# Kernel optimization log

Measured on AMD Instinct MI355X. Metric: run time of the kernel, lower is better.

Reference implementation:

```python
import jax, jax.numpy as jnp
import numpy as np

H = 64
VOCAB = 64
READ_FREQ = 16


def setup_inputs() -> dict:
    key = jax.random.key(0)
    ks = jax.random.split(key, 16)
    B, L, M = 512, 2048, 256
    seq = jax.random.randint(ks[0], (B, L), 0, VOCAB)
    memory = jax.random.normal(ks[1], (B, M, H), dtype=jnp.float32)
    s = 0.1
    return {
        "seq": seq,
        "memory": memory,
        "embed_w": jax.random.normal(ks[2], (VOCAB, H), jnp.float32) * s,
        "gru_w_ih": jax.random.normal(ks[3], (3 * H, 2 * H), jnp.float32) * s,
        "gru_w_hh": jax.random.normal(ks[4], (3 * H, H), jnp.float32) * s,
        "gru_b_ih": jax.random.normal(ks[5], (3 * H,), jnp.float32) * s,
        "gru_b_hh": jax.random.normal(ks[6], (3 * H,), jnp.float32) * s,
        "key_w": jax.random.normal(ks[7], (H, H), jnp.float32) * s,
        "key_b": jax.random.normal(ks[8], (H,), jnp.float32) * s,
        "val_w": jax.random.normal(ks[9], (H, H), jnp.float32) * s,
        "val_b": jax.random.normal(ks[10], (H,), jnp.float32) * s,
        "query_w": jax.random.normal(ks[11], (H, H), jnp.float32) * s,
        "query_b": jax.random.normal(ks[12], (H,), jnp.float32) * s,
        "head_w": jax.random.normal(ks[13], (VOCAB, H), jnp.float32) * s,
        "head_b": jax.random.normal(ks[14], (VOCAB,), jnp.float32) * s,
    }


def _forward(seq, memory, embed_w, gru_w_ih, gru_w_hh, gru_b_ih, gru_b_hh,
             key_w, key_b, val_w, val_b, query_w, query_b, head_w, head_b):
    B, L = seq.shape
    scale = 1.0 / (H ** 0.5)
    # memory is fixed: precompute keys/values once (B, M, H)
    k = jnp.einsum("bmh,kh->bmk", memory, key_w) + key_b
    v = jnp.einsum("bmh,kh->bmk", memory, val_w) + val_b
    # embed all tokens up front: (B, L, H) -> chunks (C, F, B, H)
    emb = embed_w[seq]
    C = L // READ_FREQ
    emb_chunks = emb.reshape(B, C, READ_FREQ, H).transpose(1, 2, 0, 3)

    def gru_step(carry, x_t):
        h, retrieved = carry
        inp = jnp.concatenate([x_t, retrieved], axis=-1)  # (B, 2H)
        gi = inp @ gru_w_ih.T + gru_b_ih                   # (B, 3H)
        gh = h @ gru_w_hh.T + gru_b_hh                     # (B, 3H)
        i_r, i_z, i_n = jnp.split(gi, 3, axis=-1)
        h_r, h_z, h_n = jnp.split(gh, 3, axis=-1)
        r = jax.nn.sigmoid(i_r + h_r)
        z = jax.nn.sigmoid(i_z + h_z)
        n = jnp.tanh(i_n + r * h_n)
        h_new = (1.0 - z) * n + z * h
        return (h_new, retrieved), None

    def chunk_step(h, chunk_emb):  # chunk_emb: (READ_FREQ, B, H)
        q = h @ query_w.T + query_b                        # (B, H)
        scores = jnp.einsum("bh,bmh->bm", q, k) * scale
        w = jax.nn.softmax(scores, axis=-1)
        retrieved = jnp.einsum("bm,bmh->bh", w, v)
        (h, _), _ = jax.lax.scan(gru_step, (h, retrieved), chunk_emb)
        return h, None

    h0 = jnp.zeros((B, H), dtype=memory.dtype)
    h, _ = jax.lax.scan(chunk_step, h0, emb_chunks)
    return h @ head_w.T + head_b                            # (B, VOCAB)


def reference(seq, memory, embed_w, gru_w_ih, gru_w_hh, gru_b_ih, gru_b_hh,
              key_w, key_b, val_w, val_b, query_w, query_b, head_w, head_b):
    return _forward(seq, memory, embed_w, gru_w_ih, gru_w_hh, gru_b_ih, gru_b_hh,
                    key_w, key_b, val_w, val_b, query_w, query_b, head_w, head_b)
```

## Files before the change

kernel.cpp:

```cpp
#include <hip/hip_runtime.h>
#include <hip/hip_fp16.h>


#define B_ 512
#define L_ 2048
#define M_ 256
#define H_ 64
#define C_ 128
#define F_ 16

typedef float v2f __attribute__((ext_vector_type(2)));
typedef _Float16 h2v __attribute__((ext_vector_type(2)));

#if __has_builtin(__builtin_amdgcn_fdot2)
__device__ __forceinline__ float FDOT2(h2v a, h2v b, float c) {
    return __builtin_amdgcn_fdot2(a, b, c, false);
}
#else
__device__ __forceinline__ float FDOT2(h2v a, h2v b, float c) {
    return c + (float)a[0]*(float)b[0] + (float)a[1]*(float)b[1];
}
#endif

__device__ __forceinline__ h2v bch(unsigned u) { return __builtin_bit_cast(h2v, u); }
__device__ __forceinline__ unsigned rl_u(unsigned v, int lane) {
    return (unsigned)__builtin_amdgcn_readlane((int)v, lane);
}
__device__ __forceinline__ float rl(float v, int lane) {
    return __int_as_float(__builtin_amdgcn_readlane(__float_as_int(v), lane));
}
__device__ __forceinline__ unsigned packpair(float mine, float other, bool odd) {
    float lo = odd ? other : mine;
    float hi = odd ? mine : other;
    auto r = __builtin_amdgcn_cvt_pkrtz(lo, hi);
    return __builtin_bit_cast(unsigned, r);
}
__device__ __forceinline__ float dot4(float4 a, float4 b) {
    return a.x*b.x + a.y*b.y + a.z*b.z + a.w*b.w;
}
__device__ __forceinline__ void cvt2v(uint2 raw, v2f& lo, v2f& hi) {
    __half2* hp = (__half2*)&raw;
    float2 a = __half22float2(hp[0]);
    float2 b = __half22float2(hp[1]);
    lo[0] = a.x; lo[1] = a.y; hi[0] = b.x; hi[1] = b.y;
}
__device__ __forceinline__ float fast_rcp(float x) { return __builtin_amdgcn_rcpf(x); }
__device__ __forceinline__ float sigm(float x) { return fast_rcp(1.f + __expf(-x)); }
__device__ __forceinline__ float tanh_f(float x) {
    float e2 = __expf(-2.f * fabsf(x));
    return copysignf((1.f - e2) * fast_rcp(1.f + e2), x);
}
__device__ __forceinline__ unsigned h2rn(float a, float b) {
    __half2 h = __floats2half2_rn(a, b);
    return __builtin_bit_cast(unsigned, h);
}

#define WS_KT    0u
#define WS_V     16777216u
#define WS_G     33554432u
#define WS_WPHH  33603584u
#define WS_WR    33628160u
#define WS_QP    33652736u
#define WS_KWP   33660928u
#define WS_VWP   33677312u

#define S_KT   0u
#define S_V    32768u
#define S_QP   65536u
#define S_P    73728u
#define SMEM_BYTES 74752u

__global__ void pack_weights(const float* __restrict__ w_ih,
                             const float* __restrict__ w_hh,
                             const float* __restrict__ qw,
                             const float* __restrict__ kw,
                             const float* __restrict__ vw,
                             unsigned* __restrict__ WPhh2,
                             unsigned* __restrict__ WR2p,
                             unsigned* __restrict__ QP2,
                             float4* __restrict__ KWP,
                             float4* __restrict__ VWP)
{
    int idx = blockIdx.x * 256 + threadIdx.x;
    if (idx < 6144) {
        int j = idx & 63, t = idx >> 6, g = t % 3, k2 = t / 3;
        const float* s = w_hh + (g*64 + j)*64 + 2*k2;
        WPhh2[idx] = h2rn(s[0], s[1]);
    } else if (idx < 12288) {
        int i = idx - 6144;
        int j = i & 63, t = i >> 6, g = t % 3, k2 = t / 3;
        const float* s = w_ih + (g*64 + j)*128 + 64 + 2*k2;
        WR2p[i] = h2rn(s[0], s[1]);
    } else if (idx < 14336) {
        int i = idx - 12288;
        int j = i & 63, k2 = i >> 6;
        const float* s = qw + j*64 + 2*k2;
        QP2[i] = h2rn(s[0], s[1]);
    } else if (idx < 15360) {
        int i = idx - 14336;
        int j = i & 63, k4 = i >> 6;
        const float* s = kw + j*64 + 4*k4;
        KWP[i] = make_float4(s[0], s[1], s[2], s[3]);
    } else if (idx < 16384) {
        int i = idx - 15360;
        int j = i & 63, k4 = i >> 6;
        const float* s = vw + j*64 + 4*k4;
        VWP[i] = make_float4(s[0], s[1], s[2], s[3]);
    }
}

__global__ __launch_bounds__(64) void build_G(const float* __restrict__ embed_w,
                                              const float* __restrict__ w_ih,
                                              const float* __restrict__ b_ih,
                                              float* __restrict__ G)
{
    int v = blockIdx.x, j = threadIdx.x;
    __shared__ float e_s[64];
    e_s[j] = embed_w[v*64 + j];
    __syncthreads();
    float a0 = b_ih[j], a1 = b_ih[64 + j], a2 = b_ih[128 + j];
    for (int k = 0; k < 64; ++k) {
        float e = e_s[k];
        a0 += e * w_ih[j*128 + k];
        a1 += e * w_ih[(64 + j)*128 + k];
        a2 += e * w_ih[(128 + j)*128 + k];
    }
    G[v*192 + j]       = a0;
    G[v*192 + 64 + j]  = a1;
    G[v*192 + 128 + j] = a2;
}

__global__ __launch_bounds__(256) void compute_kv(const float* __restrict__ memory,
                                                  const float* __restrict__ key_b,
                                                  const float* __restrict__ val_b,
                                                  const float4* __restrict__ KWP,
                                                  const float4* __restrict__ VWP,
                                                  unsigned* __restrict__ kT2,
                                                  __half* __restrict__ v_h)
{
    int wid = threadIdx.x >> 6;
    int o   = threadIdx.x & 63;
    int row = blockIdx.x * 4 + wid;
    int b = row >> 8, m = row & 255;
    __shared__ __align__(16) float mem_s[4][64];
    mem_s[wid][o] = memory[(size_t)row * 64 + o];
    __syncthreads();
    float ak = key_b[o], av = val_b[o];
    const float4* m4 = (const float4*)mem_s[wid];
#pragma unroll
    for (int k4 = 0; k4 < 16; ++k4) {
        float4 mm = m4[k4];
        ak += dot4(mm, KWP[k4*64 + o]);
        av += dot4(mm, VWP[k4*64 + o]);
    }
    float nb = __shfl_xor(ak, 1);
    if ((o & 1) == 0)
        kT2[((size_t)b*32 + (o >> 1))*256 + m] = h2rn(ak, nb);
    v_h[(size_t)row*64 + o] = __float2half(av);
}

#define GRU_STEP(cg0, cg1, cg2) do {                                        \
    float gr = (cg0) + RrB, gz = (cg1) + RzB, gn = bhn;                     \
    _Pragma("unroll")                                                       \
    for (int kp = 0; kp < 32; ++kp) {                                       \
        h2v hhp = bch(rl_u(hpu, 2*kp));                                     \
        gr = FDOT2(hhp, wr2[kp], gr);                                       \
        gz = FDOT2(hhp, wz2[kp], gz);                                       \
        gn = FDOT2(hhp, wn2[kp], gn);                                       \
    }                                                                       \
    float r_ = sigm(gr);                                                    \
    float z_ = sigm(gz);                                                    \
    float n_ = tanh_f(((cg2) + Rn) + r_ * gn);                              \
    h = fmaf(z_, h - n_, n_);                                               \
    float hx_ = __shfl_xor(h, 1);                                           \
    hpu = packpair(h, hx_, odd);                                            \
} while (0)

__global__ __launch_bounds__(64, 1) void recurrent_main(
    const int*   __restrict__ seq,
    const float* __restrict__ b_hh,
    const float* __restrict__ query_b,
    const float* __restrict__ head_w,
    const float* __restrict__ head_b,
    const unsigned* __restrict__ kT2g,
    const __half* __restrict__ v_h,
    const float* __restrict__ G,
    const unsigned* __restrict__ WPhh2,
    const unsigned* __restrict__ WR2p,
    const unsigned* __restrict__ QP2g,
    float* __restrict__ out)
{
    const int b = blockIdx.x;
    const int j = threadIdx.x;
    const bool odd = (j & 1);

    extern __shared__ __align__(16) char smem[];
    const uint4* kT2_lds = (const uint4*)(smem + S_KT);
    const uint2* v_u2    = (const uint2*)(smem + S_V);
    const unsigned* qp2  = (const unsigned*)(smem + S_QP);
    float4* p_s4  = (float4*)(smem + S_P);

    {
        const uint4* kTg = (const uint4*)(kT2g + (size_t)b * 8192);
        const uint4* vg  = (const uint4*)(v_h  + (size_t)b * 16384);
        uint4* kTls = (uint4*)(smem + S_KT);
        uint4* vls  = (uint4*)(smem + S_V);
#pragma unroll
        for (int i = 0; i < 32; ++i) {
            kTls[i*64 + j] = kTg[i*64 + j];
            vls[i*64 + j]  = vg[i*64 + j];
        }
        const uint4* qpg = (const uint4*)QP2g;
        uint4* qls = (uint4*)(smem + S_QP);
#pragma unroll
        for (int i = 0; i < 8; ++i) qls[i*64 + j] = qpg[i*64 + j];
    }

    h2v wr2[32], wz2[32], wn2[32];
#pragma unroll
    for (int k2 = 0; k2 < 32; ++k2) {
        wr2[k2] = bch(WPhh2[(k2*3 + 0)*64 + j]);
        wz2[k2] = bch(WPhh2[(k2*3 + 1)*64 + j]);
        wn2[k2] = bch(WPhh2[(k2*3 + 2)*64 + j]);
    }
    h2v rr2[32], rz2[32], rn2[32];
#pragma unroll
    for (int k2 = 0; k2 < 32; ++k2) {
        rr2[k2] = bch(WR2p[(k2*3 + 0)*64 + j]);
        rz2[k2] = bch(WR2p[(k2*3 + 1)*64 + j]);
        rn2[k2] = bch(WR2p[(k2*3 + 2)*64 + j]);
    }

    float h = 0.f;
    unsigned hpu = 0u;
    const float bhr = b_hh[j], bhz = b_hh[64 + j], bhn = b_hh[128 + j];
    const float qb  = query_b[j];

    const int* seqb = seq + (size_t)b * L_;
    const int o4 = j & 15;
    const int mg = j >> 4;
    __builtin_amdgcn_wave_barrier();

    for (int c = 0; c < C_; ++c) {
        const int c16 = c * F_;

        float q = qb;
#pragma unroll 8
        for (int k2 = 0; k2 < 32; ++k2) {
            h2v pp = bch(qp2[k2*64 + j]);
            h2v hh = bch(rl_u(hpu, 2*k2));
            q = FDOT2(hh, pp, q);
        }

        float qx = __shfl_xor(q, 1);
        unsigned qpu = packpair(q, qx, odd);
        float s0 = 0.f, s1 = 0.f, s2 = 0.f, s3 = 0.f;
#pragma unroll 8
        for (int t = 0; t < 32; ++t) {
            h2v qq = bch(rl_u(qpu, 2*t));
            uint4 kk = kT2_lds[t*64 + j];
            s0 = FDOT2(bch(kk.x), qq, s0);
            s1 = FDOT2(bch(kk.y), qq, s1);
            s2 = FDOT2(bch(kk.z), qq, s2);
            s3 = FDOT2(bch(kk.w), qq, s3);
        }
        const float scale = 0.125f;
        float4 p;
        p.x = __expf(s0*scale); p.y = __expf(s1*scale);
        p.z = __expf(s2*scale); p.w = __expf(s3*scale);
        float sum = (p.x + p.y) + (p.z + p.w);
#pragma unroll
        for (int o = 32; o > 0; o >>= 1) sum += __shfl_xor(sum, o);
        float inv = fast_rcp(sum);
        p_s4[j] = p;
        __builtin_amdgcn_wave_barrier();

        const float* ps = (const float*)p_s4;
        v2f aA0 = {0.f,0.f}, aB0 = {0.f,0.f};
        v2f aA1 = {0.f,0.f}, aB1 = {0.f,0.f};
#pragma unroll 4
        for (int i = 0; i < 64; i += 2) {
            int m0 = 4*i + mg, m1 = 4*(i + 1) + mg;
            float p0 = ps[m0], p1 = ps[m1];
            v2f v0l, v0h, v1l, v1h;
            cvt2v(v_u2[m0*16 + o4], v0l, v0h);
            cvt2v(v_u2[m1*16 + o4], v1l, v1h);
            aA0 += v0l * p0; aB0 += v0h * p0;
            aA1 += v1l * p1; aB1 += v1h * p1;
        }
        float4 acc;
        acc.x = (aA0[0] + aA1[0]) * inv;
        acc.y = (aA0[1] + aA1[1]) * inv;
        acc.z = (aB0[0] + aB1[0]) * inv;
        acc.w = (aB0[1] + aB1[1]) * inv;
#pragma unroll
        for (int o = 16; o <= 32; o <<= 1) {
            acc.x += __shfl_xor(acc.x, o);
            acc.y += __shfl_xor(acc.y, o);
            acc.z += __shfl_xor(acc.z, o);
            acc.w += __shfl_xor(acc.w, o);
        }

        unsigned rp0 = packpair(acc.x, acc.y, false);
        unsigned rp1 = packpair(acc.z, acc.w, false);
        float Rr = 0.f, Rz = 0.f, Rn = 0.f;
#pragma unroll
        for (int k2 = 0; k2 < 32; ++k2) {
            unsigned rsel = (k2 & 1) ? rp1 : rp0;
            h2v rr = bch(rl_u(rsel, k2 >> 1));
            Rr = FDOT2(rr, rr2[k2], Rr);
            Rz = FDOT2(rr, rz2[k2], Rz);
            Rn = FDOT2(rr, rn2[k2], Rn);
        }
        const float RrB = Rr + bhr, RzB = Rz + bhz;

#pragma unroll 1
        for (int g = 0; g < 4; ++g) {
            const int4 tg = *(const int4*)(seqb + c16 + 4*g);
            const float* GA = G + tg.x*192;
            const float* GB = G + tg.y*192;
            const float* GC = G + tg.z*192;
            const float* GD = G + tg.w*192;
            float gA0 = GA[j], gA1 = GA[64+j], gA2 = GA[128+j];
            float gB0 = GB[j], gB1 = GB[64+j], gB2 = GB[128+j];
            float gC0 = GC[j], gC1 = GC[64+j], gC2 = GC[128+j];
            float gD0 = GD[j], gD1 = GD[64+j], gD2 = GD[128+j];

            GRU_STEP(gA0, gA1, gA2);
            GRU_STEP(gB0, gB1, gB2);
            GRU_STEP(gC0, gC1, gC2);
            GRU_STEP(gD0, gD1, gD2);
        }
    }

    float o = head_b[j];
#pragma unroll
    for (int k4 = 0; k4 < 16; ++k4) {
        float h0 = rl(h, 4*k4+0), h1 = rl(h, 4*k4+1);
        float h2 = rl(h, 4*k4+2), h3 = rl(h, 4*k4+3);
        const float* hw = head_w + j*64 + 4*k4;
        o += h0*hw[0] + h1*hw[1] + h2*hw[2] + h3*hw[3];
    }
    out[(size_t)b*64 + j] = o;
}

extern "C" void kernel_launch(void* const* d_in, const int* in_sizes, int n_in,
                              void* d_out, int out_size, void* d_ws, size_t ws_size,
                              hipStream_t stream) {
    const int*   seq      = (const int*)  d_in[0];
    const float* memory   = (const float*)d_in[1];
    const float* embed_w  = (const float*)d_in[2];
    const float* w_ih     = (const float*)d_in[3];
    const float* w_hh     = (const float*)d_in[4];
    const float* b_ih     = (const float*)d_in[5];
    const float* b_hh     = (const float*)d_in[6];
    const float* key_w    = (const float*)d_in[7];
    const float* key_b    = (const float*)d_in[8];
    const float* val_w    = (const float*)d_in[9];
    const float* val_b    = (const float*)d_in[10];
    const float* query_w  = (const float*)d_in[11];
    const float* query_b  = (const float*)d_in[12];
    const float* head_w   = (const float*)d_in[13];
    const float* head_b   = (const float*)d_in[14];

    char* ws = (char*)d_ws;
    unsigned* kT2  = (unsigned*)(ws + WS_KT);
    __half*   v_h  = (__half*)  (ws + WS_V);
    float*    G    = (float*)   (ws + WS_G);
    unsigned* WPhh2 = (unsigned*)(ws + WS_WPHH);
    unsigned* WR2p  = (unsigned*)(ws + WS_WR);
    unsigned* QP2   = (unsigned*)(ws + WS_QP);
    float4*   KWP   = (float4*)  (ws + WS_KWP);
    float4*   VWP   = (float4*)  (ws + WS_VWP);

    (void)hipFuncSetAttribute((const void*)recurrent_main,
                              hipFuncAttributeMaxDynamicSharedMemorySize,
                              (int)SMEM_BYTES);

    pack_weights<<<64, 256, 0, stream>>>(w_ih, w_hh, query_w, key_w, val_w,
                                         WPhh2, WR2p, QP2, KWP, VWP);
    build_G<<<64, 64, 0, stream>>>(embed_w, w_ih, b_ih, G);
    compute_kv<<<(B_*M_)/4, 256, 0, stream>>>(memory, key_b, val_b, KWP, VWP, kT2, v_h);
    recurrent_main<<<B_, 64, SMEM_BYTES, stream>>>(seq, b_hh, query_b, head_w, head_b,
                                                   kT2, v_h, G, WPhh2, WR2p, QP2,
                                                   (float*)d_out);
}
```

Before: 1.502 ms.

## Transpose values to per-output-row fp16 pairs and use fdot2 for retrieval

Values are now stored transposed, with pairs of memory slots packed as fp16 along m for each output channel. Each lane then computes its own retrieved channel with fdot2 over 256 slots, reading a padded LDS row and a packed fp16 probability vector. This replaces the split-m accumulation that needed cross-lane shuffle reductions and fp16-to-fp32 conversions. Token indices for the chunk are also loaded up front. In exchange, probabilities lose precision by being rounded to fp16, and compute_kv gains an extra block barrier.

```diff
diff --git a/kernel.cpp b/kernel.cpp
--- a/kernel.cpp
+++ b/kernel.cpp
@@ -35,14 +35,12 @@
     auto r = __builtin_amdgcn_cvt_pkrtz(lo, hi);
     return __builtin_bit_cast(unsigned, r);
 }
+__device__ __forceinline__ unsigned pkrtz(float a, float b) {
+    auto r = __builtin_amdgcn_cvt_pkrtz(a, b);
+    return __builtin_bit_cast(unsigned, r);
+}
 __device__ __forceinline__ float dot4(float4 a, float4 b) {
     return a.x*b.x + a.y*b.y + a.z*b.z + a.w*b.w;
-}
-__device__ __forceinline__ void cvt2v(uint2 raw, v2f& lo, v2f& hi) {
-    __half2* hp = (__half2*)&raw;
-    float2 a = __half22float2(hp[0]);
-    float2 b = __half22float2(hp[1]);
-    lo[0] = a.x; lo[1] = a.y; hi[0] = b.x; hi[1] = b.y;
 }
 __device__ __forceinline__ float fast_rcp(float x) { return __builtin_amdgcn_rcpf(x); }
 __device__ __forceinline__ float sigm(float x) { return fast_rcp(1.f + __expf(-x)); }
@@ -66,9 +64,9 @@
 
 #define S_KT   0u
 #define S_V    32768u
-#define S_QP   65536u
-#define S_P    73728u
-#define SMEM_BYTES 74752u
+#define S_QP   66560u
+#define S_P    74752u
+#define SMEM_BYTES 75264u
 
 __global__ void pack_weights(const float* __restrict__ w_ih,
                              const float* __restrict__ w_hh,
@@ -136,13 +134,14 @@
                                                   const float4* __restrict__ KWP,
                                                   const float4* __restrict__ VWP,
                                                   unsigned* __restrict__ kT2,
-                                                  __half* __restrict__ v_h)
+                                                  unsigned* __restrict__ vT2)
 {
     int wid = threadIdx.x >> 6;
     int o   = threadIdx.x & 63;
     int row = blockIdx.x * 4 + wid;
     int b = row >> 8, m = row & 255;
     __shared__ __align__(16) float mem_s[4][64];
+    __shared__ float avs[4][64];
     mem_s[wid][o] = memory[(size_t)row * 64 + o];
     __syncthreads();
     float ak = key_b[o], av = val_b[o];
@@ -156,7 +155,11 @@
     float nb = __shfl_xor(ak, 1);
     if ((o & 1) == 0)
         kT2[((size_t)b*32 + (o >> 1))*256 + m] = h2rn(ak, nb);
-    v_h[(size_t)row*64 + o] = __float2half(av);
+    avs[wid][o] = av;
+    __syncthreads();
+    if ((wid & 1) == 0) {
+        vT2[((size_t)b*64 + o)*128 + (m >> 1)] = h2rn(avs[wid][o], avs[wid+1][o]);
+    }
 }
 
 #define GRU_STEP(cg0, cg1, cg2) do {                                        \
@@ -183,7 +186,7 @@
     const float* __restrict__ head_w,
     const float* __restrict__ head_b,
     const unsigned* __restrict__ kT2g,
-    const __half* __restrict__ v_h,
+    const unsigned* __restrict__ vT2g,
     const float* __restrict__ G,
     const unsigned* __restrict__ WPhh2,
     const unsigned* __restrict__ WR2p,
@@ -196,19 +199,19 @@
 
     extern __shared__ __align__(16) char smem[];
     const uint4* kT2_lds = (const uint4*)(smem + S_KT);
-    const uint2* v_u2    = (const uint2*)(smem + S_V);
     const unsigned* qp2  = (const unsigned*)(smem + S_QP);
-    float4* p_s4  = (float4*)(smem + S_P);
 
     {
         const uint4* kTg = (const uint4*)(kT2g + (size_t)b * 8192);
-        const uint4* vg  = (const uint4*)(v_h  + (size_t)b * 16384);
         uint4* kTls = (uint4*)(smem + S_KT);
-        uint4* vls  = (uint4*)(smem + S_V);
+#pragma unroll
+        for (int i = 0; i < 32; ++i) kTls[i*64 + j] = kTg[i*64 + j];
+        const uint4* vg4 = (const uint4*)(vT2g + (size_t)b * 8192);
+        uint4* vls4 = (uint4*)(smem + S_V);
 #pragma unroll
         for (int i = 0; i < 32; ++i) {
-            kTls[i*64 + j] = kTg[i*64 + j];
-            vls[i*64 + j]  = vg[i*64 + j];
+            int t = i*64 + j;
+            vls4[(t >> 5)*33 + (t & 31)] = vg4[t];
         }
         const uint4* qpg = (const uint4*)QP2g;
         uint4* qls = (uint4*)(smem + S_QP);
@@ -237,12 +240,17 @@
     const float qb  = query_b[j];
 
     const int* seqb = seq + (size_t)b * L_;
-    const int o4 = j & 15;
-    const int mg = j >> 4;
+    const uint4* vrow = (const uint4*)(smem + S_V) + j*33;
+    const uint4* p4   = (const uint4*)(smem + S_P);
     __builtin_amdgcn_wave_barrier();
 
     for (int c = 0; c < C_; ++c) {
         const int c16 = c * F_;
+
+        const int4 pA = *(const int4*)(seqb + c16);
+        const int4 pB = *(const int4*)(seqb + c16 + 4);
+        const int4 pC = *(const int4*)(seqb + c16 + 8);
+        const int4 pD = *(const int4*)(seqb + c16 + 12);
 
         float q = qb;
 #pragma unroll 8
@@ -272,42 +280,28 @@
 #pragma unroll
         for (int o = 32; o > 0; o >>= 1) sum += __shfl_xor(sum, o);
         float inv = fast_rcp(sum);
-        p_s4[j] = p;
+        *(uint2*)(smem + S_P + (size_t)j*8) =
+            make_uint2(pkrtz(p.x, p.y), pkrtz(p.z, p.w));
         __builtin_amdgcn_wave_barrier();
 
-        const float* ps = (const float*)p_s4;
-        v2f aA0 = {0.f,0.f}, aB0 = {0.f,0.f};
-        v2f aA1 = {0.f,0.f}, aB1 = {0.f,0.f};
-#pragma unroll 4
-        for (int i = 0; i < 64; i += 2) {
-            int m0 = 4*i + mg, m1 = 4*(i + 1) + mg;
-            float p0 = ps[m0], p1 = ps[m1];
-            v2f v0l, v0h, v1l, v1h;
-            cvt2v(v_u2[m0*16 + o4], v0l, v0h);
-            cvt2v(v_u2[m1*16 + o4], v1l, v1h);
-            aA0 += v0l * p0; aB0 += v0h * p0;
-            aA1 += v1l * p1; aB1 += v1h * p1;
-        }
-        float4 acc;
-        acc.x = (aA0[0] + aA1[0]) * inv;
-        acc.y = (aA0[1] + aA1[1]) * inv;
-        acc.z = (aB0[0] + aB1[0]) * inv;
-        acc.w = (aB0[1] + aB1[1]) * inv;
-#pragma unroll
-        for (int o = 16; o <= 32; o <<= 1) {
-            acc.x += __shfl_xor(acc.x, o);
-            acc.y += __shfl_xor(acc.y, o);
-            acc.z += __shfl_xor(acc.z, o);
-            acc.w += __shfl_xor(acc.w, o);
-        }
-
-        unsigned rp0 = packpair(acc.x, acc.y, false);
-        unsigned rp1 = packpair(acc.z, acc.w, false);
+        float racc = 0.f;
+#pragma unroll 8
+        for (int qd = 0; qd < 32; ++qd) {
+            uint4 vv = vrow[qd];
+            uint4 pp = p4[qd];
+            racc = FDOT2(bch(pp.x), bch(vv.x), racc);
+            racc = FDOT2(bch(pp.y), bch(vv.y), racc);
+            racc = FDOT2(bch(pp.z), bch(vv.z), racc);
+            racc = FDOT2(bch(pp.w), bch(vv.w), racc);
+        }
+        float ret = racc * inv;
+
+        float rx = __shfl_xor(ret, 1);
+        unsigned rpu = packpair(ret, rx, odd);
         float Rr = 0.f, Rz = 0.f, Rn = 0.f;
 #pragma unroll
         for (int k2 = 0; k2 < 32; ++k2) {
-            unsigned rsel = (k2 & 1) ? rp1 : rp0;
-            h2v rr = bch(rl_u(rsel, k2 >> 1));
+            h2v rr = bch(rl_u(rpu, 2*k2));
             Rr = FDOT2(rr, rr2[k2], Rr);
             Rz = FDOT2(rr, rz2[k2], Rz);
             Rn = FDOT2(rr, rn2[k2], Rn);
@@ -316,7 +310,14 @@
 
 #pragma unroll 1
         for (int g = 0; g < 4; ++g) {
-            const int4 tg = *(const int4*)(seqb + c16 + 4*g);
+            const bool gb1 = (g & 1), gb2 = (g & 2);
+            int4 tlo, thi, tg;
+            tlo.x = gb1 ? pB.x : pA.x; tlo.y = gb1 ? pB.y : pA.y;
+            tlo.z = gb1 ? pB.z : pA.z; tlo.w = gb1 ? pB.w : pA.w;
+            thi.x = gb1 ? pD.x : pC.x; thi.y = gb1 ? pD.y : pC.y;
+            thi.z = gb1 ? pD.z : pC.z; thi.w = gb1 ? pD.w : pC.w;
+            tg.x = gb2 ? thi.x : tlo.x; tg.y = gb2 ? thi.y : tlo.y;
+            tg.z = gb2 ? thi.z : tlo.z; tg.w = gb2 ? thi.w : tlo.w;
             const float* GA = G + tg.x*192;
             const float* GB = G + tg.y*192;
             const float* GC = G + tg.z*192;
@@ -365,7 +366,7 @@
 
     char* ws = (char*)d_ws;
     unsigned* kT2  = (unsigned*)(ws + WS_KT);
-    __half*   v_h  = (__half*)  (ws + WS_V);
+    unsigned* vT2  = (unsigned*)(ws + WS_V);
     float*    G    = (float*)   (ws + WS_G);
     unsigned* WPhh2 = (unsigned*)(ws + WS_WPHH);
     unsigned* WR2p  = (unsigned*)(ws + WS_WR);
@@ -380,8 +381,8 @@
     pack_weights<<<64, 256, 0, stream>>>(w_ih, w_hh, query_w, key_w, val_w,
                                          WPhh2, WR2p, QP2, KWP, VWP);
     build_G<<<64, 64, 0, stream>>>(embed_w, w_ih, b_ih, G);
-    compute_kv<<<(B_*M_)/4, 256, 0, stream>>>(memory, key_b, val_b, KWP, VWP, kT2, v_h);
+    compute_kv<<<(B_*M_)/4, 256, 0, stream>>>(memory, key_b, val_b, KWP, VWP, kT2, vT2);
     recurrent_main<<<B_, 64, SMEM_BYTES, stream>>>(seq, b_hh, query_b, head_w, head_b,
-                                                   kT2, v_h, G, WPhh2, WR2p, QP2,
+                                                   kT2, vT2, G, WPhh2, WR2p, QP2,
                                                    (float*)d_out);
 }
```

New measurement: 1.395 ms. -7.2%, faster.
